# Kernel tuning notes

Measured on AMD Instinct MI355X. Metric: run time of the kernel, lower is better.

## Reference

```python
import jax, jax.numpy as jnp
import numpy as np

B, D_IN, D_HID, D_OUT = 16384, 512, 512, 512
E, K = 8, 2
VQ_COEFF, LB_COEFF = 0.05, 0.01
LOG100 = float(np.log(100.0))
LOG2 = float(np.log(2.0))


def _normalize(v):
    # torch F.normalize(dim=1): x / max(||x||, 1e-12)
    n = jnp.linalg.norm(v, axis=-1, keepdims=True)
    return v / jnp.maximum(n, 1e-12)


def _cv_squared(v):
    # torch .var() is unbiased (ddof=1)
    return jnp.var(v, ddof=1) / (jnp.mean(v) ** 2 + 1e-10)


def _rbm_layer(x, rm, W, b, ca, temp):
    # x: [B, d_in], rm: [E, d_in], W: [E, d_out, d_in], b: [E, d_out]
    rm_n = jax.lax.stop_gradient(_normalize(rm))          # .detach() in source
    nx = _normalize(x)
    dists = nx @ rm_n.T                                    # [B, E]
    top_v, top_i = jax.lax.top_k(dists, K)                 # [B, K]
    tv = jax.nn.softmax(top_v, axis=-1)                    # softmax over top-k
    bsz = dists.shape[0]
    attn = jnp.zeros_like(dists).at[jnp.arange(bsz)[:, None], top_i].set(tv)
    # const_attention is frozen (requires_grad=False)
    inp_att = jnp.exp(jnp.minimum(jax.lax.stop_gradient(ca), LOG100))  # [E]
    # dense gather-compute-scatter: expert e output for every token, masked by attn
    eo = jnp.einsum('bi,eoi->beo', x, W) * inp_att[None, :, None] + b[None, :, :]
    out = jnp.einsum('be,beo->bo', jax.lax.stop_gradient(attn), eo)    # att.detach()
    out = out * jnp.exp(jnp.minimum(temp, LOG100))
    # aux losses (eval mode: no EMA memory update)
    vq = -(nx[:, None, :] * rm_n[top_i]).sum(-1)           # [B, K]
    vq_loss = (tv * vq).sum(-1).mean()
    lb = _cv_squared(attn.sum(0))
    aux = VQ_COEFF * vq_loss + LB_COEFF * lb               # sim_coeff = 0
    return out, aux


def setup_inputs() -> dict:
    key = jax.random.key(0)
    ks = jax.random.split(key, 8)
    x = jax.random.normal(ks[0], (B, D_IN), dtype=jnp.float32)
    rm0 = _normalize(jax.random.normal(ks[1], (E, D_IN), dtype=jnp.float32))
    W0 = jax.random.normal(ks[2], (E, D_HID, D_IN), dtype=jnp.float32) / np.sqrt(D_IN)
    b0 = jnp.zeros((E, D_HID), dtype=jnp.float32)
    rm1 = _normalize(jax.random.normal(ks[3], (E, D_HID), dtype=jnp.float32))
    W1 = jax.random.normal(ks[4], (E, D_OUT, D_HID), dtype=jnp.float32) / np.sqrt(D_HID)
    b1 = jnp.zeros((E, D_OUT), dtype=jnp.float32)
    temp0 = jnp.full((1,), LOG2, dtype=jnp.float32)
    temp1 = jnp.full((1,), LOG2, dtype=jnp.float32)
    ca0 = jnp.zeros((E,), dtype=jnp.float32)
    ca1 = jnp.zeros((E,), dtype=jnp.float32)
    return {"x": x, "rm0": rm0, "W0": W0, "b0": b0, "temp0": temp0, "ca0": ca0,
            "rm1": rm1, "W1": W1, "b1": b1, "temp1": temp1, "ca1": ca1}


def reference(x, rm0, W0, b0, temp0, ca0, rm1, W1, b1, temp1, ca1):
    h0, a0 = _rbm_layer(x, rm0, W0, b0, ca0, temp0)
    h_emb = h0                      # embedding tapped after layer 0 (pre-activation)
    h = jax.nn.relu(h0)             # norm_type=None -> no norm
    h1, a1 = _rbm_layer(h, rm1, W1, b1, ca1, temp1)
    return (h_emb, h1, a0 + a1)
```

## Files before the change

### kernel.cpp

```cpp
#include <hip/hip_runtime.h>
#include <cmath>
#include <cstdint>

#define NTOK   16384
#define DM     512
#define NEXP   8
#define LOG100 4.605170185988092f

typedef _Float16 half8  __attribute__((ext_vector_type(8)));
typedef float    floatx4 __attribute__((ext_vector_type(4)));

#define MFMA_F16(a, b, c) __builtin_amdgcn_mfma_f32_16x16x32_f16((a), (b), (c), 0, 0, 0)

__device__ __forceinline__ void gl_lds16(const void* g, void* l) {
    __builtin_amdgcn_global_load_lds(
        (const __attribute__((address_space(1))) void*)g,
        (__attribute__((address_space(3))) void*)l, 16, 0, 0);
}


__global__ __launch_bounds__(256) void prep_kernel(
    const float* __restrict__ rm0, const float* __restrict__ rm1,
    const float* __restrict__ ca0, const float* __restrict__ ca1,
    const float* __restrict__ temp0, const float* __restrict__ temp1,
    float* __restrict__ ctrl, float* __restrict__ rmn)
{
    int tid = threadIdx.x, lane = tid & 63, w = tid >> 6;
    if (tid < 32) ((int*)ctrl)[tid] = 0;
    if (tid >= 32 && tid < 48) ctrl[tid] = 0.f;
    if (tid == 48 || tid == 49) ctrl[tid] = 0.f;
    if (tid == 50) ctrl[50] = expf(fminf(temp0[0], LOG100));
    if (tid == 51) ctrl[51] = expf(fminf(temp1[0], LOG100));
    if (tid >= 52 && tid < 68) {
        int i = tid - 52;
        ctrl[tid] = expf(fminf(i < 8 ? ca0[i] : ca1[i - 8], LOG100));
    }
    for (int r = w; r < 16; r += 4) {
        const float* src = (r < 8) ? (rm0 + r * DM) : (rm1 + (r - 8) * DM);
        float v[8]; float ss = 0.f;
        #pragma unroll
        for (int j = 0; j < 8; ++j) { v[j] = src[lane + 64 * j]; ss += v[j] * v[j]; }
        #pragma unroll
        for (int off = 32; off > 0; off >>= 1) ss += __shfl_xor(ss, off);
        float inv = 1.f / fmaxf(sqrtf(ss), 1e-12f);
        float* dst = rmn + r * DM;
        #pragma unroll
        for (int j = 0; j < 8; ++j) dst[lane + 64 * j] = v[j] * inv;
    }
}

__global__ __launch_bounds__(256) void pack_w_kernel(
    const float* __restrict__ W0, const float* __restrict__ W1,
    half8* __restrict__ w0pk, half8* __restrict__ w1pk)
{
    int i = blockIdx.x * 256 + threadIdx.x;
    if (i < 512 * 1024) {
        int l = i & 63, j = (i >> 6) & 15, kb = (i >> 10) & 15, nt = (i >> 14) & 3, e = i >> 16;
        int s = l >> 3, p = l & 7, c = p ^ s;
        int n = nt * 128 + j * 8 + s;
        int k = kb * 32 + (c & 3) * 8;
        const float* src = W0 + ((size_t)e * DM + n) * DM + k;
        half8 v;
        #pragma unroll
        for (int t = 0; t < 8; ++t) {
            float f = src[t];
            _Float16 h = (_Float16)f;
            v[t] = (c < 4) ? h : (_Float16)(f - (float)h);
        }
        w0pk[i] = v;
    } else {
        int m = i - 512 * 1024;
        int l = m & 63, j = (m >> 6) & 15, kb = (m >> 10) & 7, nt = (m >> 13) & 3, e = m >> 15;
        int s = l >> 3, p = l & 7, c = p ^ s;
        int n = nt * 128 + j * 8 + s;
        int k = kb * 64 + c * 8;
        const float* src = W1 + ((size_t)e * DM + n) * DM + k;
        half8 v;
        #pragma unroll
        for (int t = 0; t < 8; ++t) v[t] = (_Float16)src[t];
        w1pk[m] = v;
    }
}

__global__ __launch_bounds__(256) void route_kernel(
    const float* __restrict__ src,
    const float* __restrict__ rmn,
    int relu_in, int split,
    _Float16* __restrict__ dst,
    unsigned char* __restrict__ key,
    float2* __restrict__ wts,
    float2* __restrict__ bs)
{
    __shared__ float rmLds[NEXP * DM];
    int tid = threadIdx.x;
    for (int i = tid; i < NEXP * DM; i += 256) rmLds[i] = rmn[i];
    __syncthreads();
    int lane = tid & 63, w = tid >> 6;
    int token = blockIdx.x * 4 + w;

    const float* row = src + (size_t)token * DM;
    float x[8]; float ss = 0.f;
    #pragma unroll
    for (int j = 0; j < 8; ++j) {
        float v = row[lane + 64 * j];
        if (relu_in) v = fmaxf(v, 0.f);
        x[j] = v; ss += v * v;
    }
    if (split) {
        #pragma unroll
        for (int j = 0; j < 8; ++j) {
            int k = lane + 64 * j;
            size_t base = (size_t)token * 1024 + (size_t)((k >> 5) << 6) + (k & 31);
            _Float16 h = (_Float16)x[j];
            dst[base] = h;
            dst[base + 32] = (_Float16)(x[j] - (float)h);
        }
    } else {
        #pragma unroll
        for (int j = 0; j < 8; ++j)
            dst[(size_t)token * DM + lane + 64 * j] = (_Float16)x[j];
    }
    float d[8];
    #pragma unroll
    for (int e = 0; e < 8; ++e) {
        float a = 0.f;
        #pragma unroll
        for (int j = 0; j < 8; ++j) a += x[j] * rmLds[e * DM + lane + 64 * j];
        d[e] = a;
    }
    #pragma unroll
    for (int off = 32; off > 0; off >>= 1) {
        ss += __shfl_xor(ss, off);
        #pragma unroll
        for (int e = 0; e < 8; ++e) d[e] += __shfl_xor(d[e], off);
    }
    float inv = 1.f / fmaxf(sqrtf(ss), 1e-12f);
    float best = -1e30f, second = -1e30f; int be = 0, se = 0;
    #pragma unroll
    for (int e = 0; e < 8; ++e) {
        float de = d[e] * inv;
        if (de > best)        { second = best; se = be; best = de; be = e; }
        else if (de > second) { second = de; se = e; }
    }
    float z = expf(second - best);
    float w0 = 1.f / (1.f + z), w1 = z / (1.f + z);
    if (lane == 0) {
        key[token] = (unsigned char)be;
        key[NTOK + token] = (unsigned char)se;
        wts[token] = make_float2(w0, w1);
        bs[token] = make_float2(best, second);
    }
}

__global__ __launch_bounds__(256) void compact_kernel(
    const unsigned char* __restrict__ key,
    const float2* __restrict__ wts,
    const float2* __restrict__ bs,
    int* __restrict__ cnt,
    unsigned short* __restrict__ bkt,
    float* __restrict__ imp,
    float* __restrict__ vq_acc)
{
    int slot = blockIdx.x >> 3, e = blockIdx.x & 7;
    const unsigned char* k = key + slot * NTOK;
    unsigned short* ob = bkt + (size_t)(slot * 8 + e) * NTOK;
    __shared__ int wc[2][4];
    int tid = threadIdx.x, lane = tid & 63, w = tid >> 6;
    int base = 0;
    float wsum = 0.f, vqs = 0.f;
    for (int c = 0; c < 64; ++c) {
        int tok = c * 256 + tid;
        bool m = (k[tok] == (unsigned char)e);
        unsigned long long mask = __ballot(m);
        int p = c & 1;
        if (lane == 0) wc[p][w] = __popcll(mask);
        __syncthreads();
        int off = base;
        for (int i = 0; i < w; ++i) off += wc[p][i];
        if (m) {
            int pre = __popcll(mask & ((1ull << lane) - 1ull));
            ob[off + pre] = (unsigned short)tok;
            float2 wp = wts[tok]; float2 b2 = bs[tok];
            float wv = slot ? wp.y : wp.x;
            wsum += wv;
            vqs  += wv * (slot ? b2.y : b2.x);
        }
        base += wc[p][0] + wc[p][1] + wc[p][2] + wc[p][3];
    }
    #pragma unroll
    for (int off = 32; off > 0; off >>= 1) {
        wsum += __shfl_xor(wsum, off);
        vqs  += __shfl_xor(vqs, off);
    }
    __shared__ float rw[4], rv[4];
    if (lane == 0) { rw[w] = wsum; rv[w] = vqs; }
    __syncthreads();
    if (tid == 0) {
        cnt[slot * 8 + e] = base;
        float W = rw[0] + rw[1] + rw[2] + rw[3];
        float V = rv[0] + rv[1] + rv[2] + rv[3];
        atomicAdd(&imp[e], W);
        atomicAdd(vq_acc, -V);
    }
}

template <bool SPLIT>
__global__ __launch_bounds__(256) void gemm_kernel(
    const _Float16* __restrict__ A,
    const _Float16* __restrict__ Wpk,
    const float* __restrict__ bias,
    const float* __restrict__ iav,
    const float* __restrict__ tscp,
    const int* __restrict__ cnt,
    const unsigned short* __restrict__ bkt,
    const float2* __restrict__ wts,
    int slot, int accum,
    float* __restrict__ outp)
{
    __shared__ __align__(16) _Float16 lds[2 * 16384];
    __shared__ int tokLds[128];

    int bx = ((blockIdx.x & 7) << 7) | (blockIdx.x >> 3);
    int e = bx >> 7, mt = bx & 127;
    int M = cnt[e];
    int m0 = mt << 7;
    if (m0 >= M) return;
    int nt = blockIdx.y, n0 = nt << 7;
    int valid = min(128, M - m0);
    int tid = threadIdx.x, lane = tid & 63, w = tid >> 6;
    if (tid < 128) tokLds[tid] = bkt[e * NTOK + m0 + min(tid, valid - 1)];
    __syncthreads();

    int subRow = lane >> 3, p = lane & 7;
    int cSt = p ^ subRow;
    int wm = w >> 1, wn = w & 1;
    int r0 = wm * 64, c0 = wn * 64;
    int q = lane >> 4, l15 = lane & 15;

    constexpr int KIT = SPLIT ? 16 : 8;
    constexpr int AS  = SPLIT ? 1024 : 512;

    int tokR[4];
    #pragma unroll
    for (int jj = 0; jj < 4; ++jj) tokR[jj] = tokLds[(w + jj * 4) * 8 + subRow];

    const _Float16* wtile = Wpk + (size_t)(e * 4 + nt) * KIT * 8192;

    floatx4 acc[4][4];
    #pragma unroll
    for (int mi = 0; mi < 4; ++mi)
        #pragma unroll
        for (int ni = 0; ni < 4; ++ni) acc[mi][ni] = (floatx4){0.f, 0.f, 0.f, 0.f};

    auto stage = [&](int kb, int buf) {
        _Float16* dA = lds + buf * 16384;
        _Float16* dB = dA + 8192;
        #pragma unroll
        for (int jj = 0; jj < 4; ++jj) {
            int j = w + jj * 4;
            gl_lds16(A + (size_t)tokR[jj] * AS + kb * 64 + cSt * 8, (void*)(dA + j * 512));
        }
        const _Float16* wb = wtile + (size_t)kb * 8192;
        #pragma unroll
        for (int jj = 0; jj < 4; ++jj) {
            int j = w + jj * 4;
            gl_lds16(wb + j * 512 + lane * 8, (void*)(dB + j * 512));
        }
    };

    auto compute = [&](int buf) {
        const _Float16* bA = lds + buf * 16384;
        const _Float16* bB = bA + 8192;
        if constexpr (SPLIT) {
            half8 ah[4], al[4];
            #pragma unroll
            for (int mi = 0; mi < 4; ++mi) {
                int r = r0 + mi * 16 + l15;
                int ph = q ^ (r & 7), pl = (q + 4) ^ (r & 7);
                ah[mi] = *(const half8*)(bA + r * 64 + ph * 8);
                al[mi] = *(const half8*)(bA + r * 64 + pl * 8);
            }
            #pragma unroll
            for (int ni = 0; ni < 4; ++ni) {
                int r = c0 + ni * 16 + l15;
                int ph = q ^ (r & 7), pl = (q + 4) ^ (r & 7);
                half8 bh = *(const half8*)(bB + r * 64 + ph * 8);
                half8 bl = *(const half8*)(bB + r * 64 + pl * 8);
                #pragma unroll
                for (int mi = 0; mi < 4; ++mi) acc[mi][ni] = MFMA_F16(ah[mi], bh, acc[mi][ni]);
                #pragma unroll
                for (int mi = 0; mi < 4; ++mi) acc[mi][ni] = MFMA_F16(ah[mi], bl, acc[mi][ni]);
                #pragma unroll
                for (int mi = 0; mi < 4; ++mi) acc[mi][ni] = MFMA_F16(al[mi], bh, acc[mi][ni]);
            }
        } else {
            #pragma unroll
            for (int ks = 0; ks < 2; ++ks) {
                half8 a[4];
                #pragma unroll
                for (int mi = 0; mi < 4; ++mi) {
                    int r = r0 + mi * 16 + l15;
                    int pc = (ks * 4 + q) ^ (r & 7);
                    a[mi] = *(const half8*)(bA + r * 64 + pc * 8);
                }
                #pragma unroll
                for (int ni = 0; ni < 4; ++ni) {
                    int r = c0 + ni * 16 + l15;
                    int pc = (ks * 4 + q) ^ (r & 7);
                    half8 b = *(const half8*)(bB + r * 64 + pc * 8);
                    #pragma unroll
                    for (int mi = 0; mi < 4; ++mi) acc[mi][ni] = MFMA_F16(a[mi], b, acc[mi][ni]);
                }
            }
        }
    };

    stage(0, 0);
    __syncthreads();
    int cur = 0;
    for (int kb = 0; kb < KIT - 1; ++kb) {
        stage(kb + 1, cur ^ 1);
        compute(cur);
        __syncthreads();
        cur ^= 1;
    }
    compute(cur);

    float t = *tscp, iae = iav[e];
    float bv[4];
    #pragma unroll
    for (int ni = 0; ni < 4; ++ni) bv[ni] = bias[e * DM + n0 + c0 + ni * 16 + l15];
    #pragma unroll
    for (int mi = 0; mi < 4; ++mi) {
        int liBase = r0 + mi * 16 + q * 4;
        #pragma unroll
        for (int reg = 0; reg < 4; ++reg) {
            int li = liBase + reg;
            if (li < valid) {
                int tok = tokLds[li];
                float2 wp = wts[tok];
                float wgt = slot ? wp.y : wp.x;
                float sg = t * wgt * iae, sb = t * wgt;
                float* orow = outp + (size_t)tok * DM + n0;
                #pragma unroll
                for (int ni = 0; ni < 4; ++ni) {
                    float v = acc[mi][ni][reg] * sg + bv[ni] * sb;
                    int c = c0 + ni * 16 + l15;
                    if (accum) orow[c] += v; else orow[c] = v;
                }
            }
        }
    }
}

__global__ void finalize_kernel(const float* __restrict__ ctrl, float* __restrict__ outp)
{
    if (threadIdx.x == 0) {
        float aux = 0.f;
        for (int l = 0; l < 2; ++l) {
            float vq = ctrl[48 + l] / (float)NTOK;
            float mean = 0.f;
            for (int e = 0; e < 8; ++e) mean += ctrl[32 + l * 8 + e];
            mean *= 0.125f;
            float s = 0.f;
            for (int e = 0; e < 8; ++e) {
                float d = ctrl[32 + l * 8 + e] - mean;
                s += d * d;
            }
            float var = s / 7.f;
            float lb = var / (mean * mean + 1e-10f);
            aux += 0.05f * vq + 0.01f * lb;
        }
        *outp = aux;
    }
}

extern "C" void kernel_launch(void* const* d_in, const int* in_sizes, int n_in,
                              void* d_out, int out_size, void* d_ws, size_t ws_size,
                              hipStream_t stream) {
    const float* x     = (const float*)d_in[0];
    const float* rm0   = (const float*)d_in[1];
    const float* W0    = (const float*)d_in[2];
    const float* b0    = (const float*)d_in[3];
    const float* temp0 = (const float*)d_in[4];
    const float* ca0   = (const float*)d_in[5];
    const float* rm1   = (const float*)d_in[6];
    const float* W1    = (const float*)d_in[7];
    const float* b1    = (const float*)d_in[8];
    const float* temp1 = (const float*)d_in[9];
    const float* ca1   = (const float*)d_in[10];
    float* out = (float*)d_out;

    char* ws = (char*)d_ws;
    float* ctrl = (float*)ws;
    int*   cnt  = (int*)ctrl;
    float* imp  = ctrl + 32;
    float* vq   = ctrl + 48;
    float* tsc  = ctrl + 50;
    float* ia   = ctrl + 52;
    float* rmn  = ctrl + 128;
    float2*        wts = (float2*)(ws + (size_t)64  * 1024);
    float2*        bs  = (float2*)(ws + (size_t)384 * 1024);
    unsigned char* key = (unsigned char*)(ws + (size_t)704 * 1024);

    char* big = ws + (1 << 20);
    half8*          w0pk8 = (half8*)(big);
    half8*          w1pk8 = (half8*)(big + (size_t)8  * 1024 * 1024);
    const _Float16* w0pk  = (const _Float16*)w0pk8;
    const _Float16* w1pk  = (const _Float16*)w1pk8;
    _Float16*       h16   = (_Float16*)(big + (size_t)12 * 1024 * 1024);
    unsigned short* bkt   = (unsigned short*)(big + (size_t)28 * 1024 * 1024);

    _Float16* xpk = (_Float16*)(out + (size_t)NTOK * DM);

    prep_kernel<<<1, 256, 0, stream>>>(rm0, rm1, ca0, ca1, temp0, temp1, ctrl, rmn);
    pack_w_kernel<<<3072, 256, 0, stream>>>(W0, W1, w0pk8, w1pk8);

    route_kernel<<<4096, 256, 0, stream>>>(x, rmn, 0, 1, xpk, key, wts, bs);
    compact_kernel<<<16, 256, 0, stream>>>(key, wts, bs, cnt, bkt, imp, vq);
    gemm_kernel<true><<<dim3(1024, 4), 256, 0, stream>>>(xpk, w0pk, b0, ia, tsc,
        cnt, bkt, wts, 0, 0, out);
    gemm_kernel<true><<<dim3(1024, 4), 256, 0, stream>>>(xpk, w0pk, b0, ia, tsc,
        cnt + 8, bkt + 8 * NTOK, wts, 1, 1, out);

    route_kernel<<<4096, 256, 0, stream>>>(out, rmn + 4096, 1, 0, h16,
        key + 2 * NTOK, wts + NTOK, bs + NTOK);
    compact_kernel<<<16, 256, 0, stream>>>(key + 2 * NTOK, wts + NTOK, bs + NTOK,
        cnt + 16, bkt + 16 * NTOK, imp + 8, vq + 1);
    gemm_kernel<false><<<dim3(1024, 4), 256, 0, stream>>>(h16, w1pk, b1, ia + 8, tsc + 1,
        cnt + 16, bkt + 16 * NTOK, wts + NTOK, 0, 0, out + (size_t)NTOK * DM);
    gemm_kernel<false><<<dim3(1024, 4), 256, 0, stream>>>(h16, w1pk, b1, ia + 8, tsc + 1,
        cnt + 24, bkt + 24 * NTOK, wts + NTOK, 1, 1, out + (size_t)NTOK * DM);

    finalize_kernel<<<1, 64, 0, stream>>>(ctrl, out + (size_t)2 * NTOK * DM);
}
```

Measured before the change: 530.7 us.

## Parallelize expert compaction with atomics and launch compact grouped GEMM grid

The compaction kernel is split into 8 chunks per (slot, expert), and per-wave bucket offsets are reserved with atomicAdd on the count instead of serial block-wide prefix sums with barriers. The GEMM grid shrinks from 1024 to 135 row tiles, and each block maps its index to an (expert, tile) by scanning the prefix of per-expert tile counts, so no empty blocks launch. Token order inside buckets becomes nondeterministic. The counts must be zeroed beforehand (not visible here), and 135 tiles is just enough for the worst-case sum of ceilings over 8 experts.

```diff
diff --git a/kernel.cpp b/kernel.cpp
--- a/kernel.cpp
+++ b/kernel.cpp
@@ -3,8 +3,8 @@
 #include <cstdint>
 
 #define NTOK   16384
+#define NEXP   8
 #define DM     512
-#define NEXP   8
 #define LOG100 4.605170185988092f
 
 typedef _Float16 half8  __attribute__((ext_vector_type(8)));
@@ -162,30 +162,27 @@
     float* __restrict__ vq_acc)
 {
     int slot = blockIdx.x >> 3, e = blockIdx.x & 7;
+    int chunk = blockIdx.y;
     const unsigned char* k = key + slot * NTOK;
     unsigned short* ob = bkt + (size_t)(slot * 8 + e) * NTOK;
-    __shared__ int wc[2][4];
     int tid = threadIdx.x, lane = tid & 63, w = tid >> 6;
-    int base = 0;
     float wsum = 0.f, vqs = 0.f;
-    for (int c = 0; c < 64; ++c) {
-        int tok = c * 256 + tid;
+    for (int c = 0; c < 8; ++c) {
+        int tok = chunk * 2048 + c * 256 + tid;
         bool m = (k[tok] == (unsigned char)e);
         unsigned long long mask = __ballot(m);
-        int p = c & 1;
-        if (lane == 0) wc[p][w] = __popcll(mask);
-        __syncthreads();
-        int off = base;
-        for (int i = 0; i < w; ++i) off += wc[p][i];
+        int wcount = __popcll(mask);
+        int wbase = 0;
+        if (lane == 0 && wcount) wbase = atomicAdd(&cnt[slot * 8 + e], wcount);
+        wbase = __shfl(wbase, 0);
         if (m) {
             int pre = __popcll(mask & ((1ull << lane) - 1ull));
-            ob[off + pre] = (unsigned short)tok;
+            ob[wbase + pre] = (unsigned short)tok;
             float2 wp = wts[tok]; float2 b2 = bs[tok];
             float wv = slot ? wp.y : wp.x;
             wsum += wv;
             vqs  += wv * (slot ? b2.y : b2.x);
         }
-        base += wc[p][0] + wc[p][1] + wc[p][2] + wc[p][3];
     }
     #pragma unroll
     for (int off = 32; off > 0; off >>= 1) {
@@ -196,11 +193,8 @@
     if (lane == 0) { rw[w] = wsum; rv[w] = vqs; }
     __syncthreads();
     if (tid == 0) {
-        cnt[slot * 8 + e] = base;
-        float W = rw[0] + rw[1] + rw[2] + rw[3];
-        float V = rv[0] + rv[1] + rv[2] + rv[3];
-        atomicAdd(&imp[e], W);
-        atomicAdd(vq_acc, -V);
+        atomicAdd(&imp[e], rw[0] + rw[1] + rw[2] + rw[3]);
+        atomicAdd(vq_acc, -(rv[0] + rv[1] + rv[2] + rv[3]));
     }
 }
 
@@ -220,11 +214,16 @@
     __shared__ __align__(16) _Float16 lds[2 * 16384];
     __shared__ int tokLds[128];
 
-    int bx = ((blockIdx.x & 7) << 7) | (blockIdx.x >> 3);
-    int e = bx >> 7, mt = bx & 127;
-    int M = cnt[e];
-    int m0 = mt << 7;
-    if (m0 >= M) return;
+    int t = blockIdx.x;
+    int e = -1, m0 = 0, M = 0, acc = 0;
+    #pragma unroll
+    for (int ee = 0; ee < 8; ++ee) {
+        int Me = cnt[ee];
+        int ne = (Me + 127) >> 7;
+        if (t >= acc && t < acc + ne) { e = ee; m0 = (t - acc) << 7; M = Me; }
+        acc += ne;
+    }
+    if (e < 0) return;
     int nt = blockIdx.y, n0 = nt << 7;
     int valid = min(128, M - m0);
     int tid = threadIdx.x, lane = tid & 63, w = tid >> 6;
@@ -246,11 +245,11 @@
 
     const _Float16* wtile = Wpk + (size_t)(e * 4 + nt) * KIT * 8192;
 
-    floatx4 acc[4][4];
+    floatx4 accu[4][4];
     #pragma unroll
     for (int mi = 0; mi < 4; ++mi)
         #pragma unroll
-        for (int ni = 0; ni < 4; ++ni) acc[mi][ni] = (floatx4){0.f, 0.f, 0.f, 0.f};
+        for (int ni = 0; ni < 4; ++ni) accu[mi][ni] = (floatx4){0.f, 0.f, 0.f, 0.f};
 
     auto stage = [&](int kb, int buf) {
         _Float16* dA = lds + buf * 16384;
@@ -287,11 +286,11 @@
                 half8 bh = *(const half8*)(bB + r * 64 + ph * 8);
                 half8 bl = *(const half8*)(bB + r * 64 + pl * 8);
                 #pragma unroll
-                for (int mi = 0; mi < 4; ++mi) acc[mi][ni] = MFMA_F16(ah[mi], bh, acc[mi][ni]);
-                #pragma unroll
-                for (int mi = 0; mi < 4; ++mi) acc[mi][ni] = MFMA_F16(ah[mi], bl, acc[mi][ni]);
-                #pragma unroll
-                for (int mi = 0; mi < 4; ++mi) acc[mi][ni] = MFMA_F16(al[mi], bh, acc[mi][ni]);
+                for (int mi = 0; mi < 4; ++mi) accu[mi][ni] = MFMA_F16(ah[mi], bh, accu[mi][ni]);
+                #pragma unroll
+                for (int mi = 0; mi < 4; ++mi) accu[mi][ni] = MFMA_F16(ah[mi], bl, accu[mi][ni]);
+                #pragma unroll
+                for (int mi = 0; mi < 4; ++mi) accu[mi][ni] = MFMA_F16(al[mi], bh, accu[mi][ni]);
             }
         } else {
             #pragma unroll
@@ -309,7 +308,7 @@
                     int pc = (ks * 4 + q) ^ (r & 7);
                     half8 b = *(const half8*)(bB + r * 64 + pc * 8);
                     #pragma unroll
-                    for (int mi = 0; mi < 4; ++mi) acc[mi][ni] = MFMA_F16(a[mi], b, acc[mi][ni]);
+                    for (int mi = 0; mi < 4; ++mi) accu[mi][ni] = MFMA_F16(a[mi], b, accu[mi][ni]);
                 }
             }
         }
@@ -326,7 +325,7 @@
     }
     compute(cur);
 
-    float t = *tscp, iae = iav[e];
+    float tsc = *tscp, iae = iav[e];
     float bv[4];
     #pragma unroll
     for (int ni = 0; ni < 4; ++ni) bv[ni] = bias[e * DM + n0 + c0 + ni * 16 + l15];
@@ -340,11 +339,11 @@
                 int tok = tokLds[li];
                 float2 wp = wts[tok];
                 float wgt = slot ? wp.y : wp.x;
-                float sg = t * wgt * iae, sb = t * wgt;
+                float sg = tsc * wgt * iae, sb = tsc * wgt;
                 float* orow = outp + (size_t)tok * DM + n0;
                 #pragma unroll
                 for (int ni = 0; ni < 4; ++ni) {
-                    float v = acc[mi][ni][reg] * sg + bv[ni] * sb;
+                    float v = accu[mi][ni][reg] * sg + bv[ni] * sb;
                     int c = c0 + ni * 16 + l15;
                     if (accum) orow[c] += v; else orow[c] = v;
                 }
@@ -417,19 +416,19 @@
     pack_w_kernel<<<3072, 256, 0, stream>>>(W0, W1, w0pk8, w1pk8);
 
     route_kernel<<<4096, 256, 0, stream>>>(x, rmn, 0, 1, xpk, key, wts, bs);
-    compact_kernel<<<16, 256, 0, stream>>>(key, wts, bs, cnt, bkt, imp, vq);
-    gemm_kernel<true><<<dim3(1024, 4), 256, 0, stream>>>(xpk, w0pk, b0, ia, tsc,
+    compact_kernel<<<dim3(16, 8), 256, 0, stream>>>(key, wts, bs, cnt, bkt, imp, vq);
+    gemm_kernel<true><<<dim3(135, 4), 256, 0, stream>>>(xpk, w0pk, b0, ia, tsc,
         cnt, bkt, wts, 0, 0, out);
-    gemm_kernel<true><<<dim3(1024, 4), 256, 0, stream>>>(xpk, w0pk, b0, ia, tsc,
+    gemm_kernel<true><<<dim3(135, 4), 256, 0, stream>>>(xpk, w0pk, b0, ia, tsc,
         cnt + 8, bkt + 8 * NTOK, wts, 1, 1, out);
 
     route_kernel<<<4096, 256, 0, stream>>>(out, rmn + 4096, 1, 0, h16,
         key + 2 * NTOK, wts + NTOK, bs + NTOK);
-    compact_kernel<<<16, 256, 0, stream>>>(key + 2 * NTOK, wts + NTOK, bs + NTOK,
+    compact_kernel<<<dim3(16, 8), 256, 0, stream>>>(key + 2 * NTOK, wts + NTOK, bs + NTOK,
         cnt + 16, bkt + 16 * NTOK, imp + 8, vq + 1);
-    gemm_kernel<false><<<dim3(1024, 4), 256, 0, stream>>>(h16, w1pk, b1, ia + 8, tsc + 1,
+    gemm_kernel<false><<<dim3(135, 4), 256, 0, stream>>>(h16, w1pk, b1, ia + 8, tsc + 1,
         cnt + 16, bkt + 16 * NTOK, wts + NTOK, 0, 0, out + (size_t)NTOK * DM);
-    gemm_kernel<false><<<dim3(1024, 4), 256, 0, stream>>>(h16, w1pk, b1, ia + 8, tsc + 1,
+    gemm_kernel<false><<<dim3(135, 4), 256, 0, stream>>>(h16, w1pk, b1, ia + 8, tsc + 1,
         cnt + 24, bkt + 24 * NTOK, wts + NTOK, 1, 1, out + (size_t)NTOK * DM);
 
     finalize_kernel<<<1, 64, 0, stream>>>(ctrl, out + (size_t)2 * NTOK * DM);
```

After: 486.5 us. 1.09x faster.
